# Optimization experiments

Hardware: AMD Instinct MI355X
Metric: run time of the kernel (lower is better)

The kernel has to match this reference:

```python
import jax, jax.numpy as jnp
import numpy as np

N_QUBITS = 12
N_LAYERS = 4


def _apply_axis(state, ax, m00, m01, m10, m11):
    """Apply per-batch 2x2 gate [[m00,m01],[m10,m11]] on axis `ax` of state.
    m** have shape (batch,); state has batch as axis 0."""
    s0 = jnp.take(state, 0, axis=ax)
    s1 = jnp.take(state, 1, axis=ax)
    b = (-1,) + (1,) * (s0.ndim - 1)
    m00 = m00.reshape(b); m01 = m01.reshape(b)
    m10 = m10.reshape(b); m11 = m11.reshape(b)
    n0 = m00 * s0 + m01 * s1
    n1 = m10 * s0 + m11 * s1
    return jnp.stack([n0, n1], axis=ax)


def _rx_mats(theta):
    c = jnp.cos(theta / 2).astype(jnp.complex64)
    s = (-1j) * jnp.sin(theta / 2).astype(jnp.complex64)
    return c, s, s, c


def _ry_mats(theta):
    c = jnp.cos(theta / 2).astype(jnp.complex64)
    s = jnp.sin(theta / 2).astype(jnp.complex64)
    return c, -s, s, c


def _rz_mats(theta):
    e = jnp.exp(-0.5j * theta.astype(jnp.complex64))
    z = jnp.zeros_like(e)
    return e, z, z, jnp.conj(e)


def _apply_1q(state, wire, mats):
    return _apply_axis(state, wire + 1, *mats)


def _apply_crx(state, ctrl, tgt, theta):
    axc = ctrl + 1
    c0 = jnp.take(state, 0, axis=axc)
    c1 = jnp.take(state, 1, axis=axc)
    # target axis inside the control-removed array
    axt = tgt if (tgt + 1) > axc else tgt + 1
    c1 = _apply_axis(c1, axt, *_rx_mats(theta))
    return jnp.stack([c0, c1], axis=axc)


def _simulate(params, inputs):
    n, L = N_QUBITS, N_LAYERS
    B = params.shape[0]
    state = jnp.zeros((B,) + (2,) * n, dtype=jnp.complex64)
    state = state.at[(slice(None),) + (0,) * n].set(1.0)
    # RY input embedding
    d = inputs.shape[-1]
    for i in range(n):
        state = _apply_1q(state, i, _ry_mats(inputs[:, i % d]))
    p = 0
    for _ in range(L):
        for i in range(n):
            state = _apply_1q(state, i, _rx_mats(params[:, p]))
            state = _apply_1q(state, i, _ry_mats(params[:, p + 1]))
            state = _apply_1q(state, i, _rz_mats(params[:, p + 2]))
            p += 3
        for i in range(n):
            state = _apply_crx(state, i, (i + 1) % n, params[:, p])
            p += 1
        for i in range(n - 1, -1, -1):
            state = _apply_crx(state, i, (i - 1) % n, params[:, p])
            p += 1
    # expectation values
    xs, ys, zs = [], [], []
    for i in range(n):
        s0 = jnp.take(state, 0, axis=i + 1).reshape(B, -1)
        s1 = jnp.take(state, 1, axis=i + 1).reshape(B, -1)
        zoff = jnp.sum(jnp.conj(s0) * s1, axis=1)
        xs.append(2.0 * jnp.real(zoff))
        ys.append(2.0 * jnp.imag(zoff))
        zs.append(jnp.sum(jnp.abs(s0) ** 2 - jnp.abs(s1) ** 2, axis=1))
    out = jnp.stack(xs + ys + zs, axis=-1)  # (batch, 3*n)
    return out.astype(jnp.float32)


def setup_inputs() -> dict:
    key = jax.random.key(0)
    k1, k2 = jax.random.split(key)
    params = jax.random.normal(k1, (1024, N_QUBITS * N_LAYERS * 5), dtype=jnp.float32)
    inputs = jax.random.normal(k2, (1024, N_QUBITS), dtype=jnp.float32)
    return {"params": params, "inputs": inputs}


def reference(params, inputs):
    return _simulate(params, inputs)
```

## Files before the change

### kernel.cpp

```cpp
#include <hip/hip_runtime.h>
#include <hip/hip_fp16.h>

#define NQ     12
#define NPARAM 240
#define BLOCK  512
#define NREG   8

typedef float v2f __attribute__((ext_vector_type(2)));
typedef unsigned int h2;
#define IDH 0x00003C00u

__device__ __forceinline__ h2 pk_cmul16(h2 a, h2 b) {
    h2 t;
    asm("v_pk_mul_f16 %0, %1, %2 op_sel:[0,0] op_sel_hi:[0,1]\n\t"
        "v_pk_fma_f16 %0, %1, %2, %0 op_sel:[1,1,0] op_sel_hi:[1,0,1] neg_lo:[1,0,0]"
        : "=&v"(t) : "v"(a), "v"(b));
    return t;
}
__device__ __forceinline__ h2 pk_cmac16(h2 t0, h2 a, h2 b) {
    h2 t;
    asm("v_pk_fma_f16 %0, %2, %3, %1 op_sel:[0,0,0] op_sel_hi:[0,1,1]\n\t"
        "v_pk_fma_f16 %0, %2, %3, %0 op_sel:[1,1,0] op_sel_hi:[1,0,1] neg_lo:[1,0,0]"
        : "=&v"(t) : "v"(t0), "v"(a), "v"(b));
    return t;
}
__device__ __forceinline__ h2 pk_crx16(h2 cs2, h2 s, h2 p) {
    h2 t;
    asm("v_pk_mul_f16 %0, %1, %2 op_sel:[0,0] op_sel_hi:[0,1]\n\t"
        "v_pk_fma_f16 %0, %1, %3, %0 op_sel:[1,1,0] op_sel_hi:[1,0,1] neg_hi:[0,1,0]"
        : "=&v"(t) : "v"(cs2), "v"(s), "v"(p));
    return t;
}
__device__ __forceinline__ v2f pk_cjmac(v2f a0, v2f s, v2f p) {
    v2f t;
    asm("v_pk_fma_f32 %0, %2, %3, %1 op_sel:[0,0,0] op_sel_hi:[0,1,1]\n\t"
        "v_pk_fma_f32 %0, %2, %3, %0 op_sel:[1,1,0] op_sel_hi:[1,0,1] neg_hi:[1,0,0]"
        : "=&v"(t) : "v"(a0), "v"(s), "v"(p));
    return t;
}

__device__ __forceinline__ h2 packh2(float x, float y) {
    return ((h2)__half_as_ushort(__float2half_rn(y)) << 16) |
           (h2)__half_as_ushort(__float2half_rn(x));
}
__device__ __forceinline__ v2f uph2(h2 u) {
    return (v2f){ __half2float(__ushort_as_half((unsigned short)(u & 0xffff))),
                  __half2float(__ushort_as_half((unsigned short)(u >> 16))) };
}


constexpr int QMAP[5][12] = {
     {  0,  1,  2,  3,  4,  10, 11,  9,  8,   5,  6,  7},
     {  5,  6,  7,  8,  9,   3,  4, 10, 11,   0,  1,  2},
     { 10, 11,  0,  9,  8,   3,  4,  5,  6,   1,  2,  7},
     {  7,  6,  5,  4,  3,   9,  8, 10, 11,   0,  1,  2},
     {  2,  1,  0, 11,  4,   3,  9,  8, 10,   5,  6,  7},
};

constexpr int posof(int m, int q) {
    for (int p = 0; p < 12; ++p) if (QMAP[m][p] == q) return p;
    return -1;
}
constexpr int ebit(int p) { return p < 3 ? 9 + p : p - 3; }
constexpr int roff(int MA, int MB, int r) {
    int off = 0;
    for (int p = 0; p < 3; ++p)
        off |= ((r >> p) & 1) << ebit(posof(MA, QMAP[MB][p]));
    return off;
}

template<int MA, int MB>
__device__ __forceinline__ int rbase(int tid) {
    int base = 0;
    #pragma unroll
    for (int p = 3; p < 12; ++p)
        base |= ((tid >> (p - 3)) & 1) << ebit(posof(MA, QMAP[MB][p]));
    return base;
}

template<int MA, int MB, int PH>
__device__ __forceinline__ void remap(h2* st, int tid, h2* bufh, int base) {
    h2* bp = bufh + PH * (NREG * BLOCK);
    #pragma unroll
    for (int r = 0; r < NREG; ++r) bp[r * BLOCK + tid] = st[r];
    __syncthreads();
    #pragma unroll
    for (int r = 0; r < NREG; ++r) st[r] = bp[base + roff(MA, MB, r)];
}

template<int LM>
__device__ __forceinline__ int lxori(int v) {
    if constexpr (LM == 1) {
        return __builtin_amdgcn_update_dpp(v, v, 0xB1, 0xF, 0xF, false);
    } else if constexpr (LM == 2) {
        return __builtin_amdgcn_update_dpp(v, v, 0x4E, 0xF, 0xF, false);
    } else if constexpr (LM == 4) {
        return __builtin_amdgcn_ds_swizzle(v, 0x101F);
    } else if constexpr (LM == 8) {
        return __builtin_amdgcn_ds_swizzle(v, 0x201F);
    } else if constexpr (LM == 16) {
        return __builtin_amdgcn_ds_swizzle(v, 0x401F);
    } else {
        return __shfl_xor(v, LM, 64);
    }
}
template<int LM>
__device__ __forceinline__ h2 lxor_h(h2 v) { return (h2)lxori<LM>((int)v); }
template<int LM>
__device__ __forceinline__ v2f lxor2(v2f v) {
    v2f p = { __int_as_float(lxori<LM>(__float_as_int(v.x))),
              __int_as_float(lxori<LM>(__float_as_int(v.y))) };
    return p;
}

__device__ __forceinline__ float wsum4(float x) {
    x += __int_as_float(__builtin_amdgcn_update_dpp(0, __float_as_int(x), 0x111, 0xF, 0xF, true));
    x += __int_as_float(__builtin_amdgcn_update_dpp(0, __float_as_int(x), 0x112, 0xF, 0xF, true));
    x += __int_as_float(__builtin_amdgcn_update_dpp(0, __float_as_int(x), 0x114, 0xF, 0xF, true));
    x += __int_as_float(__builtin_amdgcn_update_dpp(0, __float_as_int(x), 0x118, 0xF, 0xF, true));
    return x;
}

__device__ __forceinline__ float2 cmulf(float2 a, float2 b) {
    return make_float2(a.x*b.x - a.y*b.y, a.x*b.y + a.y*b.x);
}

template<int P>
__device__ __forceinline__ void apply1q(h2* st, int tid, const h2* m) {
    h2 u00 = m[0], u01 = m[1], u10 = m[2], u11 = m[3];
    if constexpr (P < 3) {
        #pragma unroll
        for (int r = 0; r < NREG; ++r) {
            if ((r >> P) & 1) continue;
            int r1 = r | (1 << P);
            h2 s0 = st[r], s1 = st[r1];
            st[r]  = pk_cmac16(pk_cmul16(u00, s0), u01, s1);
            st[r1] = pk_cmac16(pk_cmul16(u10, s0), u11, s1);
        }
    } else {
        constexpr int LM = 1 << (P - 3);
        int bit = (tid >> (P - 3)) & 1;
        h2 d = bit ? u11 : u00;
        h2 o = bit ? u10 : u01;
        #pragma unroll
        for (int r = 0; r < NREG; ++r) {
            h2 p = lxor_h<LM>(st[r]);
            st[r] = pk_cmac16(pk_cmul16(d, st[r]), o, p);
        }
    }
}

template<int PC, int PT>
__device__ __forceinline__ void fgate(h2* st, int tid, const h2* A, const h2* B) {
    h2 a00 = A[0], a01 = A[1], a10 = A[2], a11 = A[3];
    h2 b00 = B[0], b01 = B[1], b10 = B[2], b11 = B[3];
    if constexpr (PT < 3) {
        if constexpr (PC < 3) {
            #pragma unroll
            for (int r = 0; r < NREG; ++r) {
                if ((r >> PT) & 1) continue;
                const bool uB = (r >> PC) & 1;
                h2 m00 = uB ? b00 : a00, m01 = uB ? b01 : a01;
                h2 m10 = uB ? b10 : a10, m11 = uB ? b11 : a11;
                int r1 = r | (1 << PT);
                h2 s0 = st[r], s1 = st[r1];
                st[r]  = pk_cmac16(pk_cmul16(m00, s0), m01, s1);
                st[r1] = pk_cmac16(pk_cmul16(m10, s0), m11, s1);
            }
        } else {
            int cbit = (tid >> (PC - 3)) & 1;
            h2 m00 = cbit ? b00 : a00, m01 = cbit ? b01 : a01;
            h2 m10 = cbit ? b10 : a10, m11 = cbit ? b11 : a11;
            #pragma unroll
            for (int r = 0; r < NREG; ++r) {
                if ((r >> PT) & 1) continue;
                int r1 = r | (1 << PT);
                h2 s0 = st[r], s1 = st[r1];
                st[r]  = pk_cmac16(pk_cmul16(m00, s0), m01, s1);
                st[r1] = pk_cmac16(pk_cmul16(m10, s0), m11, s1);
            }
        }
    } else {
        constexpr int LM = 1 << (PT - 3);
        int tbit = (tid >> (PT - 3)) & 1;
        h2 dA = tbit ? a11 : a00, oA = tbit ? a10 : a01;
        h2 dB = tbit ? b11 : b00, oB = tbit ? b10 : b01;
        if constexpr (PC < 3) {
            #pragma unroll
            for (int r = 0; r < NREG; ++r) {
                const bool uB = (r >> PC) & 1;
                h2 d = uB ? dB : dA, o = uB ? oB : oA;
                h2 p = lxor_h<LM>(st[r]);
                st[r] = pk_cmac16(pk_cmul16(d, st[r]), o, p);
            }
        } else {
            int cbit = (tid >> (PC - 3)) & 1;
            h2 d = cbit ? dB : dA, o = cbit ? oB : oA;
            #pragma unroll
            for (int r = 0; r < NREG; ++r) {
                h2 p = lxor_h<LM>(st[r]);
                st[r] = pk_cmac16(pk_cmul16(d, st[r]), o, p);
            }
        }
    }
}

template<int PC, int PT>
__device__ __forceinline__ void applyCRX(h2* st, int tid, const h2* cs) {
    h2 cs2 = cs[0];
    if constexpr (PT < 3) {
        if constexpr (PC < 3) {
            #pragma unroll
            for (int r = 0; r < NREG; ++r) {
                if (!((r >> PC) & 1) || ((r >> PT) & 1)) continue;
                int r1 = r | (1 << PT);
                h2 s0 = st[r], s1 = st[r1];
                st[r]  = pk_crx16(cs2, s0, s1);
                st[r1] = pk_crx16(cs2, s1, s0);
            }
        } else {
            int apply = (tid >> (PC - 3)) & 1;
            h2 cse = apply ? cs2 : IDH;
            #pragma unroll
            for (int r = 0; r < NREG; ++r) {
                if ((r >> PT) & 1) continue;
                int r1 = r | (1 << PT);
                h2 s0 = st[r], s1 = st[r1];
                st[r]  = pk_crx16(cse, s0, s1);
                st[r1] = pk_crx16(cse, s1, s0);
            }
        }
    } else {
        constexpr int LM = 1 << (PT - 3);
        if constexpr (PC < 3) {
            #pragma unroll
            for (int r = 0; r < NREG; ++r) {
                if (!((r >> PC) & 1)) continue;
                h2 p = lxor_h<LM>(st[r]);
                st[r] = pk_crx16(cs2, st[r], p);
            }
        } else {
            int apply = (tid >> (PC - 3)) & 1;
            h2 cse = apply ? cs2 : IDH;
            #pragma unroll
            for (int r = 0; r < NREG; ++r) {
                h2 p = lxor_h<LM>(st[r]);
                st[r] = pk_crx16(cse, st[r], p);
            }
        }
    }
}

__global__ __launch_bounds__(BLOCK)
void qfe_kernel(const float* __restrict__ params,
                const float* __restrict__ inputs,
                float* __restrict__ out) {
    const int b    = blockIdx.x;
    const int tid  = threadIdx.x;
    const int lane = tid & 63;

    __shared__ v2f buf[NREG * BLOCK];
    h2* bufh = (h2*)buf;
    __shared__ __align__(16) h2 mA[4 * 12 * 4];
    __shared__ __align__(16) h2 mB[4 * 11 * 4];
    __shared__ __align__(16) h2 mcrx[4 * 24];
    __shared__ float  redbuf[32][36];

    float2* cs = (float2*)redbuf;
    if (tid < 240) {
        float a = params[b * NPARAM + tid] * 0.5f;
        cs[tid] = make_float2(cosf(a), sinf(a));
    } else if (tid < 252) {
        float e = inputs[b * NQ + (tid - 240)] * 0.5f;
        cs[tid] = make_float2(cosf(e), sinf(e));
    }
    __syncthreads();

    if (tid < 48) {
        int l = tid / 12, q = tid % 12;
        const float2 vx = cs[l * 60 + q * 3 + 0];
        const float2 vy = cs[l * 60 + q * 3 + 1];
        const float2 vz = cs[l * 60 + q * 3 + 2];
        float cx = vx.x, sx = vx.y;
        float cy = vy.x, sy = vy.y;
        float cz = vz.x, sz = vz.y;
        float2 a00 = make_float2( cy*cx,  sy*sx);
        float2 a01 = make_float2(-sy*cx, -cy*sx);
        float2 a10 = make_float2( sy*cx, -cy*sx);
        float2 a11 = make_float2( cy*cx, -sy*sx);
        float2 e0 = make_float2(cz, -sz);
        float2 e1 = make_float2(cz,  sz);
        float2 u00 = cmulf(e0, a00), u01 = cmulf(e0, a01);
        float2 u10 = cmulf(e1, a10), u11 = cmulf(e1, a11);
        if (l == 0) {
            float ce = cs[240 + q].x, se = cs[240 + q].y;
            float2 v00 = make_float2(u00.x*ce + u01.x*se, u00.y*ce + u01.y*se);
            float2 v01 = make_float2(-u00.x*se + u01.x*ce, -u00.y*se + u01.y*ce);
            float2 v10 = make_float2(u10.x*ce + u11.x*se, u10.y*ce + u11.y*se);
            float2 v11 = make_float2(-u10.x*se + u11.x*ce, -u10.y*se + u11.y*ce);
            u00 = v00; u01 = v01; u10 = v10; u11 = v11;
        }
        h2* m = &mA[(l * 12 + q) * 4];
        m[0] = packh2(u00.x, u00.y); m[1] = packh2(u01.x, u01.y);
        m[2] = packh2(u10.x, u10.y); m[3] = packh2(u11.x, u11.y);
    }
    if (tid >= 64 && tid < 160) {
        int k2 = tid - 64;
        int l = k2 / 24, k = k2 % 24;
        float2 v = cs[l * 60 + 36 + k];
        mcrx[l * 24 + k] = packh2(v.x, v.y);
    }
    __syncthreads();
    if (tid < 44) {
        int l = tid / 11, j = tid % 11;
        const h2* U = &mA[(l * 12 + (j + 1)) * 4];
        v2f u00 = uph2(U[0]), u01 = uph2(U[1]), u10 = uph2(U[2]), u11 = uph2(U[3]);
        v2f csv = uph2(mcrx[l * 24 + j]);
        float c = csv.x, s = csv.y;
        h2* Bm = &mB[(l * 11 + j) * 4];
        Bm[0] = packh2( c*u00.x + s*u10.y,  c*u00.y - s*u10.x);
        Bm[1] = packh2( c*u01.x + s*u11.y,  c*u01.y - s*u11.x);
        Bm[2] = packh2( s*u00.y + c*u10.x, -s*u00.x + c*u10.y);
        Bm[3] = packh2( s*u01.y + c*u11.x, -s*u01.x + c*u11.y);
    }
    __syncthreads();

    h2 st[NREG];
    #pragma unroll
    for (int r = 0; r < NREG; ++r) st[r] = 0u;
    if (tid == 0) st[0] = IDH;

    const int rb41 = rbase<4,1>(tid);
    const int rb12 = rbase<1,2>(tid);
    const int rb23 = rbase<2,3>(tid);
    const int rb34 = rbase<3,4>(tid);

    #pragma unroll 1
    for (int l = 0; l < 4; ++l) {
        const h2* ma = mA + l * 48;
        const h2* mb = mB + l * 44;
        const h2* cl = mcrx + l * 24;
        apply1q<2>(st, tid, ma + 0 * 4);
        fgate<2, 1>(st, tid, ma + 1 * 4, mb + 0 * 4);
        fgate<1, 0>(st, tid, ma + 2 * 4, mb + 1 * 4);
        fgate<0, 5>(st, tid, ma + 3 * 4, mb + 2 * 4);
        fgate<5, 4>(st, tid, ma + 4 * 4, mb + 3 * 4);
        remap<4, 1, 0>(st, tid, bufh, rb41);
        fgate<6, 0>(st, tid, ma + 5 * 4, mb + 4 * 4);
        fgate<0, 1>(st, tid, ma + 6 * 4, mb + 5 * 4);
        fgate<1, 2>(st, tid, ma + 7 * 4, mb + 6 * 4);
        fgate<2, 3>(st, tid, ma + 8 * 4, mb + 7 * 4);
        fgate<3, 4>(st, tid, ma + 9 * 4, mb + 8 * 4);
        remap<1, 2, 1>(st, tid, bufh, rb12);
        fgate<3, 0>(st, tid, ma + 10 * 4, mb + 9 * 4);
        fgate<0, 1>(st, tid, ma + 11 * 4, mb + 10 * 4);
        applyCRX<1, 2>(st, tid, cl + 11);
        applyCRX<1, 0>(st, tid, cl + 12);
        applyCRX<0, 3>(st, tid, cl + 13);
        applyCRX<3, 4>(st, tid, cl + 14);
        remap<2, 3, 0>(st, tid, bufh, rb23);
        applyCRX<6, 0>(st, tid, cl + 15);
        applyCRX<0, 1>(st, tid, cl + 16);
        applyCRX<1, 2>(st, tid, cl + 17);
        applyCRX<2, 3>(st, tid, cl + 18);
        applyCRX<3, 4>(st, tid, cl + 19);
        remap<3, 4, 1>(st, tid, bufh, rb34);
        applyCRX<5, 0>(st, tid, cl + 20);
        applyCRX<0, 1>(st, tid, cl + 21);
        applyCRX<1, 2>(st, tid, cl + 22);
        applyCRX<2, 3>(st, tid, cl + 23);
    }

    v2f stf[NREG];
    #pragma unroll
    for (int r = 0; r < NREG; ++r) stf[r] = uph2(st[r]);

    float nn[NREG];
    #pragma unroll
    for (int r = 0; r < NREG; ++r) nn[r] = stf[r].x*stf[r].x + stf[r].y*stf[r].y;
    float T  = ((nn[0]+nn[1])+(nn[2]+nn[3])) + ((nn[4]+nn[5])+(nn[6]+nn[7]));
    float Z0 = ((nn[0]-nn[1])+(nn[2]-nn[3])) + ((nn[4]-nn[5])+(nn[6]-nn[7]));
    float Z1 = ((nn[0]+nn[1])-(nn[2]+nn[3])) + ((nn[4]+nn[5])-(nn[6]+nn[7]));
    float Z2 = ((nn[0]+nn[1])+(nn[2]+nn[3])) - ((nn[4]+nn[5])+(nn[6]+nn[7]));

    __syncthreads();
    #pragma unroll
    for (int r = 0; r < NREG; ++r) buf[r * BLOCK + tid] = stf[r];
    __syncthreads();

    const int row16 = (tid >> 4);
    const bool isred = (lane & 15) == 15;
    const float Tsum = wsum4(T);

#define EXP_REG(q, B, ZV) { \
    v2f acc = {0.f, 0.f}; \
    _Pragma("unroll") \
    for (int r = 0; r < NREG; ++r) { \
        if ((r >> (B)) & 1) continue; \
        acc = pk_cjmac(acc, stf[r], stf[r | (1 << (B))]); \
    } \
    float X = wsum4(2.f*acc.x), Y = wsum4(2.f*acc.y), Z = wsum4(ZV); \
    if (isred) { redbuf[row16][(q)] = X; redbuf[row16][12+(q)] = Y; redbuf[row16][24+(q)] = Z; } }

#define EXP_DPP(q, LM, TB) { \
    v2f acc = {0.f, 0.f}; \
    _Pragma("unroll") \
    for (int r = 0; r < NREG; ++r) { \
        v2f p = lxor2<LM>(stf[r]); \
        acc = pk_cjmac(acc, stf[r], p); \
    } \
    float zs = ((tid >> (TB)) & 1) ? -1.f : 1.f; \
    float X = wsum4(acc.x), Y = wsum4(zs*acc.y), Z = wsum4(zs*T); \
    if (isred) { redbuf[row16][(q)] = X; redbuf[row16][12+(q)] = Y; redbuf[row16][24+(q)] = Z; } }

#define EXP_BUF(q, XM, TB) { \
    v2f acc = {0.f, 0.f}; \
    int pt = tid ^ (XM); \
    _Pragma("unroll") \
    for (int r = 0; r < NREG; ++r) { \
        acc = pk_cjmac(acc, stf[r], buf[r * BLOCK + pt]); \
    } \
    float zs = ((tid >> (TB)) & 1) ? -1.f : 1.f; \
    float X = wsum4(acc.x), Y = wsum4(zs*acc.y), Z = wsum4(zs*T); \
    if (isred) { redbuf[row16][(q)] = X; redbuf[row16][12+(q)] = Y; redbuf[row16][24+(q)] = Z; } }

#define EXP_BUF_HI(q, XM, TB) { \
    v2f acc = {0.f, 0.f}; \
    int pt = tid ^ (XM); \
    _Pragma("unroll") \
    for (int r = 0; r < NREG; ++r) { \
        acc = pk_cjmac(acc, stf[r], buf[r * BLOCK + pt]); \
    } \
    float zs = ((tid >> (TB)) & 1) ? -1.f : 1.f; \
    float X = wsum4(acc.x), Y = wsum4(zs*acc.y), Z = zs * Tsum; \
    if (isred) { redbuf[row16][(q)] = X; redbuf[row16][12+(q)] = Y; redbuf[row16][24+(q)] = Z; } }

    EXP_REG(2, 0, Z0)  EXP_REG(1, 1, Z1)  EXP_REG(0, 2, Z2)
    EXP_DPP(11, 1, 0)  EXP_DPP(4, 2, 1)
    EXP_BUF(3, 4, 2)   EXP_BUF(9, 8, 3)
    EXP_BUF_HI(8, 16, 4)  EXP_BUF_HI(10, 32, 5)
    EXP_BUF_HI(5, 64, 6)  EXP_BUF_HI(6, 128, 7) EXP_BUF_HI(7, 256, 8)

    __syncthreads();
    if (tid < 36) {
        float acc = 0.f;
        #pragma unroll
        for (int i = 0; i < 32; ++i) acc += redbuf[i][tid];
        out[b * 36 + tid] = acc;
    }
}

extern "C" void kernel_launch(void* const* d_in, const int* in_sizes, int n_in,
                              void* d_out, int out_size, void* d_ws, size_t ws_size,
                              hipStream_t stream) {
    const float* params = (const float*)d_in[0];
    const float* inputs = (const float*)d_in[1];
    float* out = (float*)d_out;
    qfe_kernel<<<1024, BLOCK, 0, stream>>>(params, inputs, out);
}
```

Before: 105.5 us.

## Reorder qubit-position maps to need three state remaps per layer instead of four

Replaces the five qubit-to-position maps with a three-map cycle. Gate groups are regrouped so each layer needs only three shared-memory state redistributions instead of four. The layer loop is unrolled by two, with the first layer's single-qubit gates peeled out, so the double-buffer parity alternates correctly. The expectation-value mapping is updated to the new final layout. The goal is fewer LDS exchanges and barriers, at the cost of larger code and some risk of a mapping error.

```diff
diff --git a/kernel.cpp b/kernel.cpp
--- a/kernel.cpp
+++ b/kernel.cpp
@@ -49,12 +49,10 @@
 }
 
 
-constexpr int QMAP[5][12] = {
-     {  0,  1,  2,  3,  4,  10, 11,  9,  8,   5,  6,  7},
-     {  5,  6,  7,  8,  9,   3,  4, 10, 11,   0,  1,  2},
-     { 10, 11,  0,  9,  8,   3,  4,  5,  6,   1,  2,  7},
-     {  7,  6,  5,  4,  3,   9,  8, 10, 11,   0,  1,  2},
-     {  2,  1,  0, 11,  4,   3,  9,  8, 10,   5,  6,  7},
+constexpr int QMAP[3][12] = {
+     {  1,  2,  3,  0,  4,  5,  6,  7, 11,   8,  9, 10},
+     {  8,  1,  2,  5,  6,  7,  0,  4,  9,   3, 10, 11},
+     {  9, 10, 11,  0,  4,  5,  6,  7,  8,   1,  2,  3},
 };
 
 constexpr int posof(int m, int q) {
@@ -249,6 +247,40 @@
             }
         }
     }
+}
+
+__device__ __forceinline__ void Agates(h2* st, int tid, const h2* ma, const h2* mb) {
+    apply1q<3>(st, tid, ma + 0 * 4);
+    fgate<3, 0>(st, tid, ma + 1 * 4, mb + 0 * 4);
+    fgate<0, 1>(st, tid, ma + 2 * 4, mb + 1 * 4);
+    fgate<1, 2>(st, tid, ma + 3 * 4, mb + 2 * 4);
+    fgate<2, 4>(st, tid, ma + 4 * 4, mb + 3 * 4);
+}
+__device__ __forceinline__ void DEgates(h2* st, int tid, const h2* cl) {
+    applyCRX<9, 7>(st, tid, cl + 15);
+    applyCRX<7, 6>(st, tid, cl + 16);
+    applyCRX<6, 5>(st, tid, cl + 17);
+    applyCRX<5, 4>(st, tid, cl + 18);
+    applyCRX<4, 2>(st, tid, cl + 19);
+    applyCRX<2, 1>(st, tid, cl + 20);
+    applyCRX<1, 0>(st, tid, cl + 21);
+    applyCRX<0, 3>(st, tid, cl + 22);
+    applyCRX<3, 8>(st, tid, cl + 23);
+}
+__device__ __forceinline__ void Bgates(h2* st, int tid, const h2* ma, const h2* mb) {
+    fgate<7, 3>(st, tid, ma + 5 * 4, mb + 4 * 4);
+    fgate<3, 4>(st, tid, ma + 6 * 4, mb + 5 * 4);
+    fgate<4, 5>(st, tid, ma + 7 * 4, mb + 6 * 4);
+    fgate<5, 0>(st, tid, ma + 8 * 4, mb + 7 * 4);
+    fgate<0, 8>(st, tid, ma + 9 * 4, mb + 8 * 4);
+}
+__device__ __forceinline__ void Cgates(h2* st, int tid, const h2* ma, const h2* mb, const h2* cl) {
+    fgate<0, 1>(st, tid, ma + 10 * 4, mb + 9 * 4);
+    fgate<1, 2>(st, tid, ma + 11 * 4, mb + 10 * 4);
+    applyCRX<2, 3>(st, tid, cl + 11);
+    applyCRX<2, 1>(st, tid, cl + 12);
+    applyCRX<1, 0>(st, tid, cl + 13);
+    applyCRX<0, 8>(st, tid, cl + 14);
 }
 
 __global__ __launch_bounds__(BLOCK)
@@ -330,45 +362,30 @@
     for (int r = 0; r < NREG; ++r) st[r] = 0u;
     if (tid == 0) st[0] = IDH;
 
-    const int rb41 = rbase<4,1>(tid);
+    const int rb01 = rbase<0,1>(tid);
     const int rb12 = rbase<1,2>(tid);
-    const int rb23 = rbase<2,3>(tid);
-    const int rb34 = rbase<3,4>(tid);
-
+    const int rb20 = rbase<2,0>(tid);
+
+    Agates(st, tid, mA, mB);
     #pragma unroll 1
-    for (int l = 0; l < 4; ++l) {
-        const h2* ma = mA + l * 48;
-        const h2* mb = mB + l * 44;
-        const h2* cl = mcrx + l * 24;
-        apply1q<2>(st, tid, ma + 0 * 4);
-        fgate<2, 1>(st, tid, ma + 1 * 4, mb + 0 * 4);
-        fgate<1, 0>(st, tid, ma + 2 * 4, mb + 1 * 4);
-        fgate<0, 5>(st, tid, ma + 3 * 4, mb + 2 * 4);
-        fgate<5, 4>(st, tid, ma + 4 * 4, mb + 3 * 4);
-        remap<4, 1, 0>(st, tid, bufh, rb41);
-        fgate<6, 0>(st, tid, ma + 5 * 4, mb + 4 * 4);
-        fgate<0, 1>(st, tid, ma + 6 * 4, mb + 5 * 4);
-        fgate<1, 2>(st, tid, ma + 7 * 4, mb + 6 * 4);
-        fgate<2, 3>(st, tid, ma + 8 * 4, mb + 7 * 4);
-        fgate<3, 4>(st, tid, ma + 9 * 4, mb + 8 * 4);
+    for (int ll = 0; ll < 2; ++ll) {
+        const int l0 = 2 * ll, l1 = 2 * ll + 1;
+        const h2* ma0 = mA + l0 * 48;  const h2* mb0 = mB + l0 * 44;  const h2* cl0 = mcrx + l0 * 24;
+        const h2* ma1 = mA + l1 * 48;  const h2* mb1 = mB + l1 * 44;  const h2* cl1 = mcrx + l1 * 24;
+        remap<0, 1, 0>(st, tid, bufh, rb01);
+        Bgates(st, tid, ma0, mb0);
         remap<1, 2, 1>(st, tid, bufh, rb12);
-        fgate<3, 0>(st, tid, ma + 10 * 4, mb + 9 * 4);
-        fgate<0, 1>(st, tid, ma + 11 * 4, mb + 10 * 4);
-        applyCRX<1, 2>(st, tid, cl + 11);
-        applyCRX<1, 0>(st, tid, cl + 12);
-        applyCRX<0, 3>(st, tid, cl + 13);
-        applyCRX<3, 4>(st, tid, cl + 14);
-        remap<2, 3, 0>(st, tid, bufh, rb23);
-        applyCRX<6, 0>(st, tid, cl + 15);
-        applyCRX<0, 1>(st, tid, cl + 16);
-        applyCRX<1, 2>(st, tid, cl + 17);
-        applyCRX<2, 3>(st, tid, cl + 18);
-        applyCRX<3, 4>(st, tid, cl + 19);
-        remap<3, 4, 1>(st, tid, bufh, rb34);
-        applyCRX<5, 0>(st, tid, cl + 20);
-        applyCRX<0, 1>(st, tid, cl + 21);
-        applyCRX<1, 2>(st, tid, cl + 22);
-        applyCRX<2, 3>(st, tid, cl + 23);
+        Cgates(st, tid, ma0, mb0, cl0);
+        remap<2, 0, 0>(st, tid, bufh, rb20);
+        DEgates(st, tid, cl0);
+        Agates(st, tid, ma1, mb1);
+        remap<0, 1, 1>(st, tid, bufh, rb01);
+        Bgates(st, tid, ma1, mb1);
+        remap<1, 2, 0>(st, tid, bufh, rb12);
+        Cgates(st, tid, ma1, mb1, cl1);
+        remap<2, 0, 1>(st, tid, bufh, rb20);
+        DEgates(st, tid, cl1);
+        if (ll == 0) Agates(st, tid, mA + 2 * 48, mB + 2 * 44);
     }
 
     v2f stf[NREG];
@@ -435,11 +452,11 @@
     float X = wsum4(acc.x), Y = wsum4(zs*acc.y), Z = zs * Tsum; \
     if (isred) { redbuf[row16][(q)] = X; redbuf[row16][12+(q)] = Y; redbuf[row16][24+(q)] = Z; } }
 
-    EXP_REG(2, 0, Z0)  EXP_REG(1, 1, Z1)  EXP_REG(0, 2, Z2)
-    EXP_DPP(11, 1, 0)  EXP_DPP(4, 2, 1)
-    EXP_BUF(3, 4, 2)   EXP_BUF(9, 8, 3)
-    EXP_BUF_HI(8, 16, 4)  EXP_BUF_HI(10, 32, 5)
-    EXP_BUF_HI(5, 64, 6)  EXP_BUF_HI(6, 128, 7) EXP_BUF_HI(7, 256, 8)
+    EXP_REG(1, 0, Z0)  EXP_REG(2, 1, Z1)  EXP_REG(3, 2, Z2)
+    EXP_DPP(0, 1, 0)   EXP_DPP(4, 2, 1)
+    EXP_BUF(5, 4, 2)   EXP_BUF(6, 8, 3)
+    EXP_BUF_HI(7, 16, 4)   EXP_BUF_HI(11, 32, 5)
+    EXP_BUF_HI(8, 64, 6)   EXP_BUF_HI(9, 128, 7)  EXP_BUF_HI(10, 256, 8)
 
     __syncthreads();
     if (tid < 36) {
```

Result: no change. 107.3 us (+1.8%).
